# Kernel tuning notes

Measured on AMD Instinct MI355X. Metric: run time of the kernel, lower is better.

The kernel has to match this reference:

```python
import jax, jax.numpy as jnp
import numpy as np

B, S, H, L = 64, 512, 768, 9


def setup_inputs() -> dict:
    key = jax.random.key(0)
    k0, k1, k2, k3, k4, k5, k6 = jax.random.split(key, 7)
    hidden = jax.random.normal(k0, (B, S, H), dtype=jnp.float32)
    W = jax.random.normal(k1, (L, H), dtype=jnp.float32) * 0.02
    b = jnp.zeros((L,), dtype=jnp.float32)
    start_transitions = jax.random.uniform(k2, (L,), minval=-0.1, maxval=0.1)
    end_transitions = jax.random.uniform(k3, (L,), minval=-0.1, maxval=0.1)
    transitions = jax.random.uniform(k4, (L, L), minval=-0.1, maxval=0.1)
    # variable-length sequences (position 0 always valid), like real padded batches
    lens = jax.random.randint(k5, (B,), S // 2, S + 1)
    attention_mask = jnp.arange(S)[None, :] < lens[:, None]  # (B,S) bool
    labels = jax.random.randint(k6, (B, S), 0, L).astype(jnp.int32)
    return dict(hidden=hidden, W=W, b=b, start_transitions=start_transitions,
                end_transitions=end_transitions, transitions=transitions,
                labels=labels, attention_mask=attention_mask)


def _crf_neg_log_likelihood(feats, labels, mask, start, end, trans):
    """feats (B,S,L) emissions; labels (B,S) int; mask (B,S) bool. Returns scalar mean NLL."""
    fdt = feats.dtype
    # ---- log denominator: forward algorithm as a scan over time ----
    fT = jnp.swapaxes(feats, 0, 1)  # (S,B,L)
    mT = jnp.swapaxes(mask, 0, 1)   # (S,B)
    alpha0 = start + fT[0]          # (B,L)

    def step(alpha, xs):
        f_t, m_t = xs
        # (B,L_prev,1) + (L_prev,L_next) + (B,1,L_next) -> logsumexp over prev
        new = jax.nn.logsumexp(alpha[:, :, None] + trans[None, :, :] + f_t[:, None, :], axis=1)
        return jnp.where(m_t[:, None], new, alpha), None

    alpha, _ = jax.lax.scan(step, alpha0, (fT[1:], mT[1:]))
    log_den = jax.nn.logsumexp(alpha + end, axis=1)  # (B,)

    # ---- log numerator: score of the gold path, fully vectorized ----
    emit = jnp.take_along_axis(feats, labels[..., None].astype(jnp.int32), axis=2)[..., 0]  # (B,S)
    tr = trans[labels[:, :-1], labels[:, 1:]]  # (B,S-1)
    score = start[labels[:, 0]] + emit[:, 0]
    score = score + jnp.sum((tr + emit[:, 1:]) * mask[:, 1:].astype(fdt), axis=1)
    lens = jnp.sum(mask.astype(jnp.int32), axis=1) - 1  # index of last valid token
    last_tags = jnp.take_along_axis(labels, lens[:, None], axis=1)[:, 0]
    score = score + end[last_tags]

    return jnp.mean(log_den - score)


def reference(hidden, W, b, start_transitions, end_transitions, transitions, labels, attention_mask):
    # hidden2label linear (dropout is identity in eval mode)
    feats = jnp.einsum('bsh,lh->bsl', hidden, W) + b  # (B,S,L)
    return _crf_neg_log_likelihood(feats, labels, attention_mask,
                                   start_transitions, end_transitions, transitions)
```

## Files before the change

### kernel.cpp

```cpp
#include <hip/hip_runtime.h>
#include <hip/hip_bf16.h>

#define BB 64
#define SS 512
#define HH 768
#define LL 9
#define CL 16
#define NC (SS / CL)
#define NEG (-1e30f)

#if __has_builtin(__builtin_amdgcn_exp2f)
#define EXP2F(x) __builtin_amdgcn_exp2f(x)
#else
#define EXP2F(x) exp2f(x)
#endif
#if __has_builtin(__builtin_amdgcn_logf)
#define LOG2F(x) __builtin_amdgcn_logf(x)
#else
#define LOG2F(x) __log2f(x)
#endif

static __device__ __forceinline__ float dot4(float4 a, float4 b) {
    return a.x * b.x + a.y * b.y + a.z * b.z + a.w * b.w;
}

static __device__ __forceinline__ float max9(const float* v) {
    float m1 = fmaxf(fmaxf(v[0], v[1]), v[2]);
    float m2 = fmaxf(fmaxf(v[3], v[4]), v[5]);
    float m3 = fmaxf(fmaxf(v[6], v[7]), v[8]);
    return fmaxf(fmaxf(m1, m2), m3);
}

__global__ __launch_bounds__(256, 2)
void feats_kernel(const float* __restrict__ hidden,
                  const float* __restrict__ W,
                  const float* __restrict__ bias,
                  float* __restrict__ feats) {
    const int lane = threadIdx.x & 63;
    const int wv   = threadIdx.x >> 6;
    const int gw   = blockIdx.x * (blockDim.x >> 6) + wv;
    const int nw   = gridDim.x * (blockDim.x >> 6);

    float4 wreg[3][LL];
#pragma unroll
    for (int c = 0; c < 3; ++c)
#pragma unroll
        for (int l = 0; l < LL; ++l)
            wreg[c][l] = *(const float4*)(W + l * HH + c * 256 + (lane << 2));

    const float bv = bias[lane < LL ? lane : 0];

    const int R = BB * SS;
    for (int row = gw; row < R; row += nw) {
        const float4* hrow = (const float4*)(hidden + (size_t)row * HH);
        float4 h0 = hrow[lane];
        float4 h1 = hrow[64 + lane];
        float4 h2 = hrow[128 + lane];
        float acc[LL];
#pragma unroll
        for (int l = 0; l < LL; ++l)
            acc[l] = dot4(h0, wreg[0][l]) + dot4(h1, wreg[1][l]) + dot4(h2, wreg[2][l]);
#pragma unroll
        for (int l = 0; l < LL; ++l) {
            float v = acc[l];
#pragma unroll
            for (int off = 1; off < 64; off <<= 1)
                v += __shfl_xor(v, off);
            acc[l] = v;
        }
        float out = 0.f;
#pragma unroll
        for (int l = 0; l < LL; ++l)
            if (lane == l) out = acc[l];
        if (lane < LL)
            feats[(size_t)row * LL + lane] = out + bv;
    }
}

__global__ __launch_bounds__(192, 2)
void crf_chunk_kernel(const float* __restrict__ feats,
                      const float* __restrict__ trans,
                      const int* __restrict__ mask,
                      float* __restrict__ Q) {
    const float INV_LN2 = 1.4426950408889634f;
    const int b   = blockIdx.x / NC;
    const int c   = blockIdx.x % NC;
    const int tid = threadIdx.x;
    const int i   = tid >> 4;
    const int j   = tid & 15;
    const int jc  = j < LL ? j : LL - 1;

    float trC[LL];
#pragma unroll
    for (int k = 0; k < LL; ++k) trC[k] = trans[k * LL + jc] * INV_LN2;

    const int t0    = (c == 0) ? 1 : c * CL;
    const int steps = (c + 1) * CL - t0;

    const float* fb = feats + (size_t)b * SS * LL;
    const int*   mb = mask + b * SS;

    float fs[CL];
    int   na = 0;
#pragma unroll
    for (int s = 0; s < CL; ++s) {
        if (s < steps) {
            const int t = t0 + s;
            fs[s] = fb[t * LL + jc] * INV_LN2;
            na += (mb[t] != 0) ? 1 : 0;
        } else {
            fs[s] = 0.f;
        }
    }

    float P = (i == j) ? 0.f : NEG;

    for (int s = 0; s < na; ++s) {
        float v[LL];
#pragma unroll
        for (int k = 0; k < LL; ++k)
            v[k] = __shfl(P, ((i & 3) << 4) | k) + trC[k];
        const float mx = max9(v);
        float sum = 0.f;
#pragma unroll
        for (int k = 0; k < LL; ++k) sum += EXP2F(v[k] - mx);
        P = mx + LOG2F(sum) + fs[s];
    }

    if (i < LL && j < LL)
        Q[((size_t)(b * NC + c)) * (LL * LL) + i * LL + j] = P;
}

__global__ __launch_bounds__(64, 1)
void crf_combine_kernel(const float* __restrict__ feats,
                        const float* __restrict__ Q,
                        const float* __restrict__ start_t,
                        const float* __restrict__ end_t,
                        const float* __restrict__ trans,
                        const int* __restrict__ labels,
                        const int* __restrict__ mask,
                        float* __restrict__ nll_out) {
    const int b    = blockIdx.x;
    const int lane = threadIdx.x;
    const int j    = lane < LL ? lane : LL - 1;
    const float INV_LN2 = 1.4426950408889634f;
    const float LN2     = 0.6931471805599453f;

    const float* fb = feats + (size_t)b * SS * LL;
    const int*   lb = labels + b * SS;
    const int*   mb = mask + b * SS;
    const float* Qb = Q + (size_t)b * NC * (LL * LL);

    float partial = 0.f;
    int   cnt     = 0;
    for (int t = lane; t < SS; t += 64) {
        const int m = mb[t];
        cnt += (m != 0);
        if (t >= 1 && m) {
            const int lp = lb[t - 1], lc = lb[t];
            partial += trans[lp * LL + lc] + fb[t * LL + lc];
        }
    }
#pragma unroll
    for (int off = 1; off < 64; off <<= 1) {
        partial += __shfl_xor(partial, off);
        cnt     += __shfl_xor(cnt, off);
    }

    float alpha[LL];
#pragma unroll
    for (int k = 0; k < LL; ++k) alpha[k] = (start_t[k] + fb[k]) * INV_LN2;

    float qcol[LL], qnext[LL];
#pragma unroll
    for (int k = 0; k < LL; ++k) qnext[k] = Qb[k * LL + j];
    for (int c = 0; c < NC; ++c) {
#pragma unroll
        for (int k = 0; k < LL; ++k) qcol[k] = qnext[k];
        if (c + 1 < NC) {
            const float* Qn = Qb + (size_t)(c + 1) * (LL * LL);
#pragma unroll
            for (int k = 0; k < LL; ++k) qnext[k] = Qn[k * LL + j];
        }
        float v[LL];
#pragma unroll
        for (int k = 0; k < LL; ++k) v[k] = alpha[k] + qcol[k];
        const float mx = max9(v);
        float sum = 0.f;
#pragma unroll
        for (int k = 0; k < LL; ++k) sum += EXP2F(v[k] - mx);
        const float anew = mx + LOG2F(sum);
#pragma unroll
        for (int k = 0; k < LL; ++k)
            alpha[k] = __uint_as_float(__builtin_amdgcn_readlane(__float_as_uint(anew), k));
    }

    float v[LL];
#pragma unroll
    for (int k = 0; k < LL; ++k) v[k] = alpha[k] + end_t[k] * INV_LN2;
    const float mx = max9(v);
    float sum = 0.f;
#pragma unroll
    for (int k = 0; k < LL; ++k) sum += EXP2F(v[k] - mx);
    const float log_den = (mx + LOG2F(sum)) * LN2;

    if (lane == 0) {
        const int l0 = lb[0];
        const float score = start_t[l0] + fb[l0] + partial + end_t[lb[cnt - 1]];
        nll_out[b] = log_den - score;
    }
}

__global__ __launch_bounds__(64, 1)
void mean_kernel(const float* __restrict__ nll, float* __restrict__ out) {
    float v = nll[threadIdx.x];
#pragma unroll
    for (int off = 1; off < 64; off <<= 1)
        v += __shfl_xor(v, off);
    if (threadIdx.x == 0) out[0] = v * (1.0f / BB);
}

extern "C" void kernel_launch(void* const* d_in, const int* in_sizes, int n_in,
                              void* d_out, int out_size, void* d_ws, size_t ws_size,
                              hipStream_t stream) {
    const float* hidden = (const float*)d_in[0];
    const float* W      = (const float*)d_in[1];
    const float* bias   = (const float*)d_in[2];
    const float* startT = (const float*)d_in[3];
    const float* endT   = (const float*)d_in[4];
    const float* trans  = (const float*)d_in[5];
    const int*   labels = (const int*)d_in[6];
    const int*   mask   = (const int*)d_in[7];

    float* feats = (float*)d_ws;
    float* nll   = feats + (size_t)BB * SS * LL;
    float* Q     = nll + 64;

    feats_kernel<<<dim3(1024), dim3(256), 0, stream>>>(hidden, W, bias, feats);
    crf_chunk_kernel<<<dim3(BB * NC), dim3(192), 0, stream>>>(feats, trans, mask, Q);
    crf_combine_kernel<<<dim3(BB), dim3(64), 0, stream>>>(feats, Q, startT, endT, trans, labels, mask, nll);
    mean_kernel<<<dim3(1), dim3(64), 0, stream>>>(nll, (float*)d_out);
}
```

Before: 202.3 us.

## Use DPP reductions, 2-row feats loop, LDS chunk scan, and fuse mean via atomic

Feats kernel now handles two rows per iteration and reduces the dot products with DPP row ops plus two cross-row shuffles. The chunk scan exchanges P through double-buffered shared memory with block barriers instead of wave shuffles, and it raises the occupancy hint. The mean kernel is removed: the combine kernel atomically adds scaled NLL into the output, which feats_kernel zeroes. The change also swaps the AMD exp2/log builtins for generic functions, which may cost extra instructions, and the atomic makes summation order nondeterministic.

```diff
diff --git a/kernel.cpp b/kernel.cpp
--- a/kernel.cpp
+++ b/kernel.cpp
@@ -9,16 +9,8 @@
 #define NC (SS / CL)
 #define NEG (-1e30f)
 
-#if __has_builtin(__builtin_amdgcn_exp2f)
-#define EXP2F(x) __builtin_amdgcn_exp2f(x)
-#else
 #define EXP2F(x) exp2f(x)
-#endif
-#if __has_builtin(__builtin_amdgcn_logf)
-#define LOG2F(x) __builtin_amdgcn_logf(x)
-#else
 #define LOG2F(x) __log2f(x)
-#endif
 
 static __device__ __forceinline__ float dot4(float4 a, float4 b) {
     return a.x * b.x + a.y * b.y + a.z * b.z + a.w * b.w;
@@ -31,15 +23,41 @@
     return fmaxf(fmaxf(m1, m2), m3);
 }
 
+static __device__ __forceinline__ float sum9exp(const float* v, float mx) {
+    float e0 = EXP2F(v[0] - mx), e1 = EXP2F(v[1] - mx), e2 = EXP2F(v[2] - mx);
+    float e3 = EXP2F(v[3] - mx), e4 = EXP2F(v[4] - mx), e5 = EXP2F(v[5] - mx);
+    float e6 = EXP2F(v[6] - mx), e7 = EXP2F(v[7] - mx), e8 = EXP2F(v[8] - mx);
+    return ((e0 + e1) + (e2 + e3)) + (((e4 + e5) + (e6 + e7)) + e8);
+}
+
+template <int CTRL>
+static __device__ __forceinline__ float dpp_add(float v) {
+    return v + __int_as_float(
+        __builtin_amdgcn_update_dpp(0, __float_as_int(v), CTRL, 0xF, 0xF, true));
+}
+
+static __device__ __forceinline__ float wave_sum64(float v) {
+    v = dpp_add<0xB1>(v);
+    v = dpp_add<0x4E>(v);
+    v = dpp_add<0x124>(v);
+    v = dpp_add<0x128>(v);
+    v += __shfl_xor(v, 16);
+    v += __shfl_xor(v, 32);
+    return v;
+}
+
 __global__ __launch_bounds__(256, 2)
 void feats_kernel(const float* __restrict__ hidden,
                   const float* __restrict__ W,
                   const float* __restrict__ bias,
-                  float* __restrict__ feats) {
+                  float* __restrict__ feats,
+                  float* __restrict__ out0) {
+    if (blockIdx.x == 0 && threadIdx.x == 0) out0[0] = 0.f;
+
     const int lane = threadIdx.x & 63;
     const int wv   = threadIdx.x >> 6;
-    const int gw   = blockIdx.x * (blockDim.x >> 6) + wv;
-    const int nw   = gridDim.x * (blockDim.x >> 6);
+    const int gw   = blockIdx.x * 4 + wv;
+    const int nw   = 4096;
 
     float4 wreg[3][LL];
 #pragma unroll
@@ -50,38 +68,39 @@
 
     const float bv = bias[lane < LL ? lane : 0];
 
-    const int R = BB * SS;
-    for (int row = gw; row < R; row += nw) {
-        const float4* hrow = (const float4*)(hidden + (size_t)row * HH);
-        float4 h0 = hrow[lane];
-        float4 h1 = hrow[64 + lane];
-        float4 h2 = hrow[128 + lane];
-        float acc[LL];
-#pragma unroll
-        for (int l = 0; l < LL; ++l)
-            acc[l] = dot4(h0, wreg[0][l]) + dot4(h1, wreg[1][l]) + dot4(h2, wreg[2][l]);
+    for (int r0 = gw; r0 < BB * SS; r0 += 2 * nw) {
+        const int r1 = r0 + nw;
+        const float4* h0p = (const float4*)(hidden + (size_t)r0 * HH);
+        const float4* h1p = (const float4*)(hidden + (size_t)r1 * HH);
+        float4 a0 = h0p[lane], a1 = h0p[64 + lane], a2 = h0p[128 + lane];
+        float4 b0 = h1p[lane], b1 = h1p[64 + lane], b2 = h1p[128 + lane];
+
+        float accA[LL], accB[LL];
 #pragma unroll
         for (int l = 0; l < LL; ++l) {
-            float v = acc[l];
-#pragma unroll
-            for (int off = 1; off < 64; off <<= 1)
-                v += __shfl_xor(v, off);
-            acc[l] = v;
-        }
-        float out = 0.f;
-#pragma unroll
-        for (int l = 0; l < LL; ++l)
-            if (lane == l) out = acc[l];
-        if (lane < LL)
-            feats[(size_t)row * LL + lane] = out + bv;
-    }
-}
-
-__global__ __launch_bounds__(192, 2)
+            accA[l] = dot4(a0, wreg[0][l]) + dot4(a1, wreg[1][l]) + dot4(a2, wreg[2][l]);
+            accB[l] = dot4(b0, wreg[0][l]) + dot4(b1, wreg[1][l]) + dot4(b2, wreg[2][l]);
+        }
+        float outA = 0.f, outB = 0.f;
+#pragma unroll
+        for (int l = 0; l < LL; ++l) {
+            float sA = wave_sum64(accA[l]);
+            float sB = wave_sum64(accB[l]);
+            if (lane == l) { outA = sA; outB = sB; }
+        }
+        if (lane < LL) {
+            feats[(size_t)r0 * LL + lane] = outA + bv;
+            feats[(size_t)r1 * LL + lane] = outB + bv;
+        }
+    }
+}
+
+__global__ __launch_bounds__(192, 6)
 void crf_chunk_kernel(const float* __restrict__ feats,
                       const float* __restrict__ trans,
                       const int* __restrict__ mask,
                       float* __restrict__ Q) {
+    __shared__ float Pb[2][12][16];
     const float INV_LN2 = 1.4426950408889634f;
     const int b   = blockIdx.x / NC;
     const int c   = blockIdx.x % NC;
@@ -114,17 +133,22 @@
     }
 
     float P = (i == j) ? 0.f : NEG;
-
-    for (int s = 0; s < na; ++s) {
-        float v[LL];
-#pragma unroll
-        for (int k = 0; k < LL; ++k)
-            v[k] = __shfl(P, ((i & 3) << 4) | k) + trC[k];
-        const float mx = max9(v);
-        float sum = 0.f;
-#pragma unroll
-        for (int k = 0; k < LL; ++k) sum += EXP2F(v[k] - mx);
-        P = mx + LOG2F(sum) + fs[s];
+    Pb[0][i][j] = P;
+    __syncthreads();
+
+#pragma unroll
+    for (int s = 0; s < CL; ++s) {
+        if (s < na) {
+            const float* row = &Pb[s & 1][i][0];
+            float v[LL];
+#pragma unroll
+            for (int k = 0; k < LL; ++k) v[k] = row[k] + trC[k];
+            const float mx  = max9(v);
+            const float sum = sum9exp(v, mx);
+            P = mx + LOG2F(sum) + fs[s];
+            Pb[(s + 1) & 1][i][j] = P;
+        }
+        __syncthreads();
     }
 
     if (i < LL && j < LL)
@@ -139,7 +163,7 @@
                         const float* __restrict__ trans,
                         const int* __restrict__ labels,
                         const int* __restrict__ mask,
-                        float* __restrict__ nll_out) {
+                        float* __restrict__ out) {
     const int b    = blockIdx.x;
     const int lane = threadIdx.x;
     const int j    = lane < LL ? lane : LL - 1;
@@ -185,10 +209,8 @@
         float v[LL];
 #pragma unroll
         for (int k = 0; k < LL; ++k) v[k] = alpha[k] + qcol[k];
-        const float mx = max9(v);
-        float sum = 0.f;
-#pragma unroll
-        for (int k = 0; k < LL; ++k) sum += EXP2F(v[k] - mx);
+        const float mx  = max9(v);
+        const float sum = sum9exp(v, mx);
         const float anew = mx + LOG2F(sum);
 #pragma unroll
         for (int k = 0; k < LL; ++k)
@@ -198,26 +220,15 @@
     float v[LL];
 #pragma unroll
     for (int k = 0; k < LL; ++k) v[k] = alpha[k] + end_t[k] * INV_LN2;
-    const float mx = max9(v);
-    float sum = 0.f;
-#pragma unroll
-    for (int k = 0; k < LL; ++k) sum += EXP2F(v[k] - mx);
+    const float mx  = max9(v);
+    const float sum = sum9exp(v, mx);
     const float log_den = (mx + LOG2F(sum)) * LN2;
 
     if (lane == 0) {
         const int l0 = lb[0];
         const float score = start_t[l0] + fb[l0] + partial + end_t[lb[cnt - 1]];
-        nll_out[b] = log_den - score;
-    }
-}
-
-__global__ __launch_bounds__(64, 1)
-void mean_kernel(const float* __restrict__ nll, float* __restrict__ out) {
-    float v = nll[threadIdx.x];
-#pragma unroll
-    for (int off = 1; off < 64; off <<= 1)
-        v += __shfl_xor(v, off);
-    if (threadIdx.x == 0) out[0] = v * (1.0f / BB);
+        atomicAdd(out, (log_den - score) * (1.0f / BB));
+    }
 }
 
 extern "C" void kernel_launch(void* const* d_in, const int* in_sizes, int n_in,
@@ -233,11 +244,10 @@
     const int*   mask   = (const int*)d_in[7];
 
     float* feats = (float*)d_ws;
-    float* nll   = feats + (size_t)BB * SS * LL;
-    float* Q     = nll + 64;
-
-    feats_kernel<<<dim3(1024), dim3(256), 0, stream>>>(hidden, W, bias, feats);
+    float* Q     = feats + (size_t)BB * SS * LL;
+
+    feats_kernel<<<dim3(1024), dim3(256), 0, stream>>>(hidden, W, bias, feats, (float*)d_out);
     crf_chunk_kernel<<<dim3(BB * NC), dim3(192), 0, stream>>>(feats, trans, mask, Q);
-    crf_combine_kernel<<<dim3(BB), dim3(64), 0, stream>>>(feats, Q, startT, endT, trans, labels, mask, nll);
-    mean_kernel<<<dim3(1), dim3(64), 0, stream>>>(nll, (float*)d_out);
-}
+    crf_combine_kernel<<<dim3(BB), dim3(64), 0, stream>>>(feats, Q, startT, endT, trans,
+                                                          labels, mask, (float*)d_out);
+}
```

Result: no change. 203.4 us (+0.6%).
